# Kernel tuning notes

Measured on AMD Instinct MI355X. Metric: run time of the kernel, lower is better.

The kernel has to match this reference:

```python
import jax, jax.numpy as jnp
import numpy as np

B, C, H, W = 4, 64, 128, 128
KH, KW = 5, 5
PAD = 2
HEADS, DIM_HEAD = 8, 8


def setup_inputs() -> dict:
    key = jax.random.key(0)
    k1, k2, k3, k4 = jax.random.split(key, 4)
    return {
        "features1": jax.random.normal(k1, (B, C, H, W), dtype=jnp.float32),
        "features2": jax.random.normal(k2, (B, C, H, W), dtype=jnp.float32),
        "rel_h": jax.random.normal(k3, (C // 2, 1, 1, KH, 1), dtype=jnp.float32),
        "rel_w": jax.random.normal(k4, (C // 2, 1, 1, 1, KW), dtype=jnp.float32),
    }


def reference(features1, features2, rel_h, rel_w):
    b, c, h, w = features1.shape
    K = KH * KW
    # pad key/value source spatially
    padded = jnp.pad(features2, ((0, 0), (0, 0), (PAD, PAD), (PAD, PAD)))
    # materialize sliding windows: [B, C, H, W, KH*KW], kw index minor (matches torch unfold(2).unfold(3))
    windows = jnp.stack(
        [padded[:, :, i:i + h, j:j + w] for i in range(KH) for j in range(KW)],
        axis=-1,
    )
    # relative position bias: first C/2 channels get rel_h, last C/2 get rel_w
    relh = jnp.broadcast_to(rel_h.reshape(c // 2, KH, 1), (c // 2, KH, KW))
    relw = jnp.broadcast_to(rel_w.reshape(c // 2, 1, KW), (c // 2, KH, KW))
    rel = jnp.concatenate([relh, relw], axis=0).reshape(c, K)  # [C, K]
    k = windows + rel[None, :, None, None, :]
    v = windows
    q = features1.reshape(b, HEADS, DIM_HEAD, h, w, 1)
    k = k.reshape(b, HEADS, DIM_HEAD, h, w, K)
    v = v.reshape(b, HEADS, DIM_HEAD, h, w, K)
    # per-channel windowed softmax attention (no reduction over channel in scores)
    attn = jax.nn.softmax(q * k, axis=-1)
    # einsum 'abcdef,abcdef->acbde' from torch: output is [B, dim_head, heads, H, W]
    out = jnp.einsum('bhcxyk,bhcxyk->bchxy', attn, v)
    return out.reshape(b, c, h, w)
```

## Files before the change

kernel.cpp:

```cpp
#include <hip/hip_runtime.h>

#define B_ 4
#define C_ 64
#define H_ 128
#define W_ 128
#define LOG2E 1.44269504088896340736f

template<int HALF>
__device__ __forceinline__ void sa_body(int x0, int y0,
    const float* __restrict__ f1p, const float* __restrict__ f2p,
    const float* __restrict__ relp, float* __restrict__ outp)
{
    float rel5[5];
    #pragma unroll
    for (int k = 0; k < 5; ++k) rel5[k] = relp[k];

    const float mL = (x0 > 0) ? 1.0f : 0.0f;
    const float mR = (x0 < W_ - 4) ? 1.0f : 0.0f;
    const int eM = (x0 >= 4) ? x0 - 4 : 0;
    const int eP = (x0 <= W_ - 8) ? x0 + 4 : W_ - 4;

    float w[6][8];
    #pragma unroll
    for (int t = 0; t < 6; ++t) {
        const int ky = y0 + t - 2;
        const int kycl = ky < 0 ? 0 : (ky > H_ - 1 ? H_ - 1 : ky);
        const float rv = ((unsigned)ky < (unsigned)H_) ? 1.0f : 0.0f;
        const float* rp = f2p + kycl * W_;
        const float4 qm = *(const float4*)(rp + eM);
        const float4 q0 = *(const float4*)(rp + x0);
        const float4 qp = *(const float4*)(rp + eP);
        const float mLr = mL * rv, mRr = mR * rv;
        w[t][0] = qm.z * mLr; w[t][1] = qm.w * mLr;
        w[t][2] = q0.x * rv;  w[t][3] = q0.y * rv;
        w[t][4] = q0.z * rv;  w[t][5] = q0.w * rv;
        w[t][6] = qp.x * mRr; w[t][7] = qp.y * mRr;
    }

    #pragma unroll
    for (int r = 0; r < 2; ++r) {
        const float4 q4 = *(const float4*)(f1p + (y0 + r) * W_ + x0);
        const float qarr[4] = {q4.x, q4.y, q4.z, q4.w};
        float res[4];

        #pragma unroll
        for (int xo = 0; xo < 4; ++xo) {
            const float q2 = qarr[xo] * LOG2E;
            float pr[5];
            #pragma unroll
            for (int k = 0; k < 5; ++k) pr[k] = q2 * rel5[k];

            float s0 = 0.f, s1 = 0.f, d0 = 0.f, d1 = 0.f;
            #pragma unroll
            for (int i = 0; i < 5; ++i) {
                const float* row = w[r + i];
                #pragma unroll
                for (int j = 0; j < 5; ++j) {
                    const float v = row[xo + j];
                    const float p = __builtin_amdgcn_exp2f(
                        __builtin_fmaf(q2, v, pr[HALF ? j : i]));
                    if ((j & 1) == 0) { s0 += p; d0 = __builtin_fmaf(p, v, d0); }
                    else              { s1 += p; d1 = __builtin_fmaf(p, v, d1); }
                }
            }
            res[xo] = (d0 + d1) * __builtin_amdgcn_rcpf(s0 + s1);
        }

        *(float4*)(outp + (y0 + r) * W_ + x0) = (float4){res[0], res[1], res[2], res[3]};
    }
}

__global__ __launch_bounds__(256) void sa_kernel(
    const float* __restrict__ f1, const float* __restrict__ f2,
    const float* __restrict__ relh, const float* __restrict__ relw,
    float* __restrict__ out)
{
    const int tid = threadIdx.x;
    const int xq  = tid & 31;
    const int ys  = tid >> 5;
    const int blk = blockIdx.x;
    const int yb  = blk & 7;
    const int bc  = blk >> 3;
    const int c   = bc & (C_ - 1);
    const int b   = bc >> 6;
    const int x0  = xq << 2;
    const int y0  = yb * 16 + ys * 2;

    const size_t img = (size_t)(b * C_ + c) * (H_ * W_);
    const float* f1p = f1 + img;
    const float* f2p = f2 + img;

    const int c_out = (c & 7) * 8 + (c >> 3);
    float* outp = out + (size_t)(b * C_ + c_out) * (H_ * W_);

    if (c < C_ / 2) sa_body<0>(x0, y0, f1p, f2p, relh + c * 5, outp);
    else            sa_body<1>(x0, y0, f1p, f2p, relw + (c - C_ / 2) * 5, outp);
}

extern "C" void kernel_launch(void* const* d_in, const int* in_sizes, int n_in,
                              void* d_out, int out_size, void* d_ws, size_t ws_size,
                              hipStream_t stream) {
    const float* f1   = (const float*)d_in[0];
    const float* f2   = (const float*)d_in[1];
    const float* relh = (const float*)d_in[2];
    const float* relw = (const float*)d_in[3];
    float* out = (float*)d_out;

    const int grid = B_ * C_ * 8;
    sa_kernel<<<grid, 256, 0, stream>>>(f1, f2, relh, relw, out);
}
```

Before: 24.44 us.

## Pack two non-adjacent output rows into float2 lanes for packed FMA math

Each thread now handles rows y and y+8 instead of two adjacent rows, holding the window values as 2-wide float vectors so the score FMA, the sum and the weighted accumulation can use packed fp32 instructions (v_pk_fma_f32 on CDNA3/4). Because the two rows no longer overlap, each thread loads 10 key rows instead of 6, which raises global/cache load traffic. The exp2 count is unchanged, so any gain depends on whether the packed FMAs outweigh the extra loads and any register-pressure change.

```diff
diff --git a/kernel.cpp b/kernel.cpp
--- a/kernel.cpp
+++ b/kernel.cpp
@@ -6,8 +6,10 @@
 #define W_ 128
 #define LOG2E 1.44269504088896340736f
 
+typedef float v2f __attribute__((ext_vector_type(2)));
+
 template<int HALF>
-__device__ __forceinline__ void sa_body(int x0, int y0,
+__device__ __forceinline__ void sa_body(int x0, int yA, int yB,
     const float* __restrict__ f1p, const float* __restrict__ f2p,
     const float* __restrict__ relp, float* __restrict__ outp)
 {
@@ -20,54 +22,73 @@
     const int eM = (x0 >= 4) ? x0 - 4 : 0;
     const int eP = (x0 <= W_ - 8) ? x0 + 4 : W_ - 4;
 
-    float w[6][8];
+    v2f wp[5][8];
     #pragma unroll
-    for (int t = 0; t < 6; ++t) {
-        const int ky = y0 + t - 2;
-        const int kycl = ky < 0 ? 0 : (ky > H_ - 1 ? H_ - 1 : ky);
-        const float rv = ((unsigned)ky < (unsigned)H_) ? 1.0f : 0.0f;
-        const float* rp = f2p + kycl * W_;
-        const float4 qm = *(const float4*)(rp + eM);
-        const float4 q0 = *(const float4*)(rp + x0);
-        const float4 qp = *(const float4*)(rp + eP);
-        const float mLr = mL * rv, mRr = mR * rv;
-        w[t][0] = qm.z * mLr; w[t][1] = qm.w * mLr;
-        w[t][2] = q0.x * rv;  w[t][3] = q0.y * rv;
-        w[t][4] = q0.z * rv;  w[t][5] = q0.w * rv;
-        w[t][6] = qp.x * mRr; w[t][7] = qp.y * mRr;
+    for (int t = 0; t < 5; ++t) {
+        {
+            const int ky = yA + t - 2;
+            const int kycl = ky < 0 ? 0 : (ky > H_ - 1 ? H_ - 1 : ky);
+            const float rv = ((unsigned)ky < (unsigned)H_) ? 1.0f : 0.0f;
+            const float* rp = f2p + kycl * W_;
+            const float4 qm = *(const float4*)(rp + eM);
+            const float4 q0 = *(const float4*)(rp + x0);
+            const float4 qp = *(const float4*)(rp + eP);
+            const float mLr = mL * rv, mRr = mR * rv;
+            wp[t][0].x = qm.z * mLr; wp[t][1].x = qm.w * mLr;
+            wp[t][2].x = q0.x * rv;  wp[t][3].x = q0.y * rv;
+            wp[t][4].x = q0.z * rv;  wp[t][5].x = q0.w * rv;
+            wp[t][6].x = qp.x * mRr; wp[t][7].x = qp.y * mRr;
+        }
+        {
+            const int ky = yB + t - 2;
+            const int kycl = ky < 0 ? 0 : (ky > H_ - 1 ? H_ - 1 : ky);
+            const float rv = ((unsigned)ky < (unsigned)H_) ? 1.0f : 0.0f;
+            const float* rp = f2p + kycl * W_;
+            const float4 qm = *(const float4*)(rp + eM);
+            const float4 q0 = *(const float4*)(rp + x0);
+            const float4 qp = *(const float4*)(rp + eP);
+            const float mLr = mL * rv, mRr = mR * rv;
+            wp[t][0].y = qm.z * mLr; wp[t][1].y = qm.w * mLr;
+            wp[t][2].y = q0.x * rv;  wp[t][3].y = q0.y * rv;
+            wp[t][4].y = q0.z * rv;  wp[t][5].y = q0.w * rv;
+            wp[t][6].y = qp.x * mRr; wp[t][7].y = qp.y * mRr;
+        }
     }
 
+    const float4 qA4 = *(const float4*)(f1p + yA * W_ + x0);
+    const float4 qB4 = *(const float4*)(f1p + yB * W_ + x0);
+    const float qAa[4] = {qA4.x, qA4.y, qA4.z, qA4.w};
+    const float qBa[4] = {qB4.x, qB4.y, qB4.z, qB4.w};
+    float resA[4], resB[4];
+
     #pragma unroll
-    for (int r = 0; r < 2; ++r) {
-        const float4 q4 = *(const float4*)(f1p + (y0 + r) * W_ + x0);
-        const float qarr[4] = {q4.x, q4.y, q4.z, q4.w};
-        float res[4];
+    for (int xo = 0; xo < 4; ++xo) {
+        const v2f q2 = { qAa[xo] * LOG2E, qBa[xo] * LOG2E };
 
+        v2f pr[5];
         #pragma unroll
-        for (int xo = 0; xo < 4; ++xo) {
-            const float q2 = qarr[xo] * LOG2E;
-            float pr[5];
+        for (int k = 0; k < 5; ++k) pr[k] = q2 * rel5[k];
+
+        v2f s0 = {0.f,0.f}, s1 = {0.f,0.f}, d0 = {0.f,0.f}, d1 = {0.f,0.f};
+        #pragma unroll
+        for (int i = 0; i < 5; ++i) {
             #pragma unroll
-            for (int k = 0; k < 5; ++k) pr[k] = q2 * rel5[k];
+            for (int j = 0; j < 5; ++j) {
+                const v2f v  = wp[i][xo + j];
+                const v2f sc = __builtin_elementwise_fma(v, q2, pr[HALF ? j : i]);
+                const v2f p  = { __builtin_amdgcn_exp2f(sc.x),
+                                 __builtin_amdgcn_exp2f(sc.y) };
+                if (((i * 5 + j) & 1) == 0) { s0 += p; d0 = __builtin_elementwise_fma(p, v, d0); }
+                else                        { s1 += p; d1 = __builtin_elementwise_fma(p, v, d1); }
+            }
+        }
+        const v2f st = s0 + s1, dt = d0 + d1;
+        resA[xo] = dt.x * __builtin_amdgcn_rcpf(st.x);
+        resB[xo] = dt.y * __builtin_amdgcn_rcpf(st.y);
+    }
 
-            float s0 = 0.f, s1 = 0.f, d0 = 0.f, d1 = 0.f;
-            #pragma unroll
-            for (int i = 0; i < 5; ++i) {
-                const float* row = w[r + i];
-                #pragma unroll
-                for (int j = 0; j < 5; ++j) {
-                    const float v = row[xo + j];
-                    const float p = __builtin_amdgcn_exp2f(
-                        __builtin_fmaf(q2, v, pr[HALF ? j : i]));
-                    if ((j & 1) == 0) { s0 += p; d0 = __builtin_fmaf(p, v, d0); }
-                    else              { s1 += p; d1 = __builtin_fmaf(p, v, d1); }
-                }
-            }
-            res[xo] = (d0 + d1) * __builtin_amdgcn_rcpf(s0 + s1);
-        }
-
-        *(float4*)(outp + (y0 + r) * W_ + x0) = (float4){res[0], res[1], res[2], res[3]};
-    }
+    *(float4*)(outp + yA * W_ + x0) = (float4){resA[0], resA[1], resA[2], resA[3]};
+    *(float4*)(outp + yB * W_ + x0) = (float4){resB[0], resB[1], resB[2], resB[3]};
 }
 
 __global__ __launch_bounds__(256) void sa_kernel(
@@ -84,7 +105,8 @@
     const int c   = bc & (C_ - 1);
     const int b   = bc >> 6;
     const int x0  = xq << 2;
-    const int y0  = yb * 16 + ys * 2;
+    const int yA  = yb * 16 + ys;
+    const int yB  = yA + 8;
 
     const size_t img = (size_t)(b * C_ + c) * (H_ * W_);
     const float* f1p = f1 + img;
@@ -93,8 +115,8 @@
     const int c_out = (c & 7) * 8 + (c >> 3);
     float* outp = out + (size_t)(b * C_ + c_out) * (H_ * W_);
 
-    if (c < C_ / 2) sa_body<0>(x0, y0, f1p, f2p, relh + c * 5, outp);
-    else            sa_body<1>(x0, y0, f1p, f2p, relw + (c - C_ / 2) * 5, outp);
+    if (c < C_ / 2) sa_body<0>(x0, yA, yB, f1p, f2p, relh + c * 5, outp);
+    else            sa_body<1>(x0, yA, yB, f1p, f2p, relw + (c - C_ / 2) * 5, outp);
 }
 
 extern "C" void kernel_launch(void* const* d_in, const int* in_sizes, int n_in,
```

Measured after the change: 24.08 us. No clear change (-1.5%).
